# Kernel optimization log

Hardware: AMD Instinct MI355X
Metric: run time of the kernel (lower is better)

Reference implementation:

```python
import jax, jax.numpy as jnp
import numpy as np

C = 1024
H = 16
DH = C // H
T = 2048
B = 2
EPS = 1e-5


def setup_inputs() -> dict:
    key = jax.random.key(0)
    ks = jax.random.split(key, 11)
    s = 1.0 / np.sqrt(C)
    return {
        "x": jax.random.normal(ks[0], (B, C, T), dtype=jnp.float32),
        "Wq": jax.random.normal(ks[1], (C, C), dtype=jnp.float32) * s,
        "bq": jax.random.normal(ks[2], (C,), dtype=jnp.float32) * 0.01,
        "Wk": jax.random.normal(ks[3], (C, C), dtype=jnp.float32) * s,
        "bk": jax.random.normal(ks[4], (C,), dtype=jnp.float32) * 0.01,
        "Wv": jax.random.normal(ks[5], (C, C), dtype=jnp.float32) * s,
        "bv": jax.random.normal(ks[6], (C,), dtype=jnp.float32) * 0.01,
        "Wo": jax.random.normal(ks[7], (C, C), dtype=jnp.float32) * s,
        "bo": jax.random.normal(ks[8], (C,), dtype=jnp.float32) * 0.01,
        "gamma": jax.random.normal(ks[9], (C,), dtype=jnp.float32) * 0.1,
        "beta": jax.random.normal(ks[10], (C,), dtype=jnp.float32) * 0.1,
    }


def reference(x, Wq, bq, Wk, bk, Wv, bv, Wo, bo, gamma, beta):
    scale = DH ** (-0.5)
    # conv1x1 projections: [B,C,T] x [C_out,C_in] -> [B,C,T]
    q = jnp.einsum('bct,dc->bdt', x, Wq) + bq[None, :, None]
    k = jnp.einsum('bct,dc->bdt', x, Wk) + bk[None, :, None]
    v = jnp.einsum('bct,dc->bdt', x, Wv) + bv[None, :, None]
    # split heads: [B,C,T] -> [B,H,Dh,T]
    q = q.reshape(B, H, DH, T).transpose(0, 1, 3, 2) * scale  # [B,H,T,Dh]
    k = k.reshape(B, H, DH, T)                                # [B,H,Dh,T]
    v = v.reshape(B, H, DH, T).transpose(0, 1, 3, 2)          # [B,H,T,Dh]
    sim = jnp.einsum('bhtd,bhds->bhts', q, k)                 # [B,H,T,T]
    attn = jax.nn.softmax(sim, axis=-1)
    attn = jnp.nan_to_num(attn, nan=0.0)
    out = jnp.einsum('bhts,bhsd->bhtd', attn, v)              # [B,H,T,Dh]
    out = out.transpose(0, 1, 3, 2).reshape(B, C, T)          # [B,C,T]
    y = jnp.einsum('bct,dc->bdt', out, Wo) + bo[None, :, None]
    # BatchNorm1d (training mode: batch statistics over B and T)
    mean = jnp.mean(y, axis=(0, 2), keepdims=True)
    var = jnp.var(y, axis=(0, 2), keepdims=True)
    y = (y - mean) * jax.lax.rsqrt(var + EPS)
    y = y * gamma[None, :, None] + beta[None, :, None]
    return x + y
```

## Files before the change

kernel.cpp:

```cpp
#include <hip/hip_runtime.h>

#define CC 1024
#define HH 16
#define DHH 64
#define TT 2048
#define BB 2

typedef short s8v __attribute__((ext_vector_type(8)));
typedef float f32x4 __attribute__((ext_vector_type(4)));
typedef float f32x16 __attribute__((ext_vector_type(16)));

__device__ __forceinline__ unsigned short f2bf(float f) {
    union { float f; unsigned int u; } v; v.f = f;
    unsigned int r = v.u + 0x7FFFu + ((v.u >> 16) & 1u);
    return (unsigned short)(r >> 16);
}

__device__ __forceinline__ float fexp2(float x) {
#if __has_builtin(__builtin_amdgcn_exp2f)
    return __builtin_amdgcn_exp2f(x);
#else
    return exp2f(x);
#endif
}

__device__ __forceinline__ void gl_lds16(const unsigned short* g, unsigned short* l) {
    __builtin_amdgcn_global_load_lds(
        (const __attribute__((address_space(1))) unsigned int*)g,
        (__attribute__((address_space(3))) unsigned int*)l, 16, 0, 0);
}

__device__ __forceinline__ s8v lds_ld(const unsigned short* base, int byteoff) {
    return *(const s8v*)((const char*)base + byteoff);
}

__device__ __forceinline__ int xcd_swz(int orig, int nwg) {
    int cpx = nwg >> 3;
    return (orig & 7) * cpx + (orig >> 3);
}

__global__ void transpose_cast(const float* __restrict__ x, unsigned short* __restrict__ xT) {
    __shared__ float tile[32][33];
    int b = blockIdx.z;
    int t0 = blockIdx.x * 32, c0 = blockIdx.y * 32;
    int tx = threadIdx.x, ty = threadIdx.y;
    const float* xb = x + (size_t)b * CC * TT;
    #pragma unroll
    for (int i = 0; i < 32; i += 8)
        tile[ty + i][tx] = xb[(size_t)(c0 + ty + i) * TT + t0 + tx];
    __syncthreads();
    unsigned short* xTb = xT + (size_t)b * TT * CC;
    #pragma unroll
    for (int i = 0; i < 32; i += 8)
        xTb[(size_t)(t0 + ty + i) * CC + c0 + tx] = f2bf(tile[tx][ty + i]);
}

__global__ void cast_weights(const float* __restrict__ Wq, const float* __restrict__ Wk,
                             const float* __restrict__ Wv, const float* __restrict__ Wo,
                             unsigned short* __restrict__ out) {
    int i = blockIdx.x * 256 + threadIdx.x;
    int which = i >> 18;
    int j = (i & 0x3FFFF) * 4;
    const float* s = (which == 0) ? Wq : (which == 1) ? Wk : (which == 2) ? Wv : Wo;
    float4 v = *(const float4*)(s + j);
    unsigned short* d = out + (size_t)which * 1048576 + j;
    ushort4 pk; pk.x = f2bf(v.x); pk.y = f2bf(v.y); pk.z = f2bf(v.z); pk.w = f2bf(v.w);
    *(ushort4*)d = pk;
}

template<int NFRAG>
__device__ __forceinline__ void gemm_core_k1024(
    const unsigned short* __restrict__ A, const unsigned short* __restrict__ Bt,
    unsigned short* As, unsigned short* Bs,
    int m0, int n0, int tid, f32x4 (&acc)[4][NFRAG]) {
    const int w = tid >> 6, l = tid & 63;
    const int ln = l & 15, hi = l >> 4;
    const int wm = (w >> 1) * 64, wn = (w & 1) * (NFRAG * 16);
    const int BSZ = NFRAG * 1024;
    int offA[4], offB[NFRAG];
    #pragma unroll
    for (int i = 0; i < 4; ++i) {
        int ra = wm + 16 * i + ln;
        offA[i] = ra * 64 + ((hi ^ ((ra >> 1) & 3)) * 16);
    }
    #pragma unroll
    for (int j = 0; j < NFRAG; ++j) {
        int rb = wn + 16 * j + ln;
        offB[j] = rb * 64 + ((hi ^ ((rb >> 1) & 3)) * 16);
    }
    const unsigned short* ap[2];
    const unsigned short* bp[NFRAG / 2];
    #pragma unroll
    for (int j = 0; j < 2; ++j) {
        int p = j * 256 + tid;
        int r = p >> 2, g = (p & 3) ^ ((r >> 1) & 3);
        ap[j] = A + (size_t)(m0 + r) * CC + 8 * g;
    }
    #pragma unroll
    for (int j = 0; j < NFRAG / 2; ++j) {
        int p = j * 256 + tid;
        int r = p >> 2, g = (p & 3) ^ ((r >> 1) & 3);
        bp[j] = Bt + (size_t)(n0 + r) * CC + 8 * g;
    }
    auto stage = [&](int buf) {
        #pragma unroll
        for (int j = 0; j < 2; ++j) {
            gl_lds16(ap[j], As + buf * 4096 + (j * 256 + w * 64) * 8);
            ap[j] += 32;
        }
        #pragma unroll
        for (int j = 0; j < NFRAG / 2; ++j) {
            gl_lds16(bp[j], Bs + buf * BSZ + (j * 256 + w * 64) * 8);
            bp[j] += 32;
        }
    };
    stage(0); stage(1); stage(2);
    if constexpr (NFRAG == 4) asm volatile("s_waitcnt vmcnt(8)" ::: "memory");
    else                      asm volatile("s_waitcnt vmcnt(6)" ::: "memory");
    __builtin_amdgcn_sched_barrier(0);
    __builtin_amdgcn_s_barrier();
    __builtin_amdgcn_sched_barrier(0);
    int buf = 0;
    for (int kk = 0; kk < 32; ++kk) {
        const unsigned short* Ab = As + buf * 4096;
        const unsigned short* Bb = Bs + buf * BSZ;
        s8v a[4], bb[NFRAG];
        #pragma unroll
        for (int i = 0; i < 4; ++i) a[i] = lds_ld(Ab, offA[i]);
        #pragma unroll
        for (int j = 0; j < NFRAG; ++j) bb[j] = lds_ld(Bb, offB[j]);
        __builtin_amdgcn_s_setprio(1);
        #pragma unroll
        for (int i = 0; i < 4; ++i)
            #pragma unroll
            for (int jj = 0; jj < NFRAG; ++jj)
                acc[i][jj] = __builtin_amdgcn_mfma_f32_16x16x32_bf16(a[i], bb[jj], acc[i][jj], 0, 0, 0);
        __builtin_amdgcn_s_setprio(0);
        if (kk < 31) {
            if (kk < 29) {
                if constexpr (NFRAG == 4) asm volatile("s_waitcnt vmcnt(4)" ::: "memory");
                else                      asm volatile("s_waitcnt vmcnt(3)" ::: "memory");
            } else {
                asm volatile("s_waitcnt vmcnt(0)" ::: "memory");
            }
            __builtin_amdgcn_sched_barrier(0);
            __builtin_amdgcn_s_barrier();
            __builtin_amdgcn_sched_barrier(0);
            if (kk < 29) stage(buf);
            buf = (buf == 2) ? 0 : buf + 1;
        }
    }
}

__global__ __launch_bounds__(256, 3)
void gemm_qkv(const unsigned short* __restrict__ xT, const unsigned short* __restrict__ Wb,
              unsigned short* __restrict__ qTp, unsigned short* __restrict__ kTp,
              unsigned short* __restrict__ vp,
              const float* __restrict__ bq, const float* __restrict__ bk,
              const float* __restrict__ bv, float qscale) {
    __shared__ unsigned short As[3 * 4096];
    __shared__ unsigned short Bs[3 * 4096];
    const int tid = threadIdx.x;
    const int wgid = xcd_swz(blockIdx.x, 768);
    const int z = wgid >> 7, bx = wgid & 127;
    const int which = z >> 1, b = z & 1;
    const long TC = (long)TT * CC;

    const unsigned short* A; const unsigned short* Bt;
    int m0, n0;
    if (which < 2) {
        A = xT + (size_t)b * TC;
        Bt = Wb + (size_t)which * 1048576;
        n0 = (bx & 7) * 128; m0 = (bx >> 3) * 128;
    } else {
        A = Wb + 2097152;
        Bt = xT + (size_t)b * TC;
        n0 = (bx & 15) * 128; m0 = (bx >> 4) * 128;
    }

    f32x4 acc[4][4] = {};
    gemm_core_k1024<4>(A, Bt, As, Bs, m0, n0, tid, acc);

    const int w = tid >> 6, l = tid & 63;
    const int ln = l & 15, hi = l >> 4;
    const int wm = (w >> 1) * 64, wn = (w & 1) * 64;

    if (which < 2) {
        unsigned short* Out = (which == 0 ? qTp : kTp) + (size_t)b * TC;
        const float* bias = (which == 0) ? bq : bk;
        float scale = (which == 0) ? qscale : 1.0f;
        #pragma unroll
        for (int i = 0; i < 4; ++i)
            #pragma unroll
            for (int jj = 0; jj < 4; ++jj) {
                int col = n0 + wn + 16 * jj + ln;
                float bvv = bias[col];
                #pragma unroll
                for (int r = 0; r < 4; ++r) {
                    int row = m0 + wm + 16 * i + hi * 4 + r;
                    Out[(size_t)row * CC + col] = f2bf((acc[i][jj][r] + bvv) * scale);
                }
            }
    } else {
        unsigned short* Out = vp + (size_t)b * TC;
        #pragma unroll
        for (int i = 0; i < 4; ++i)
            #pragma unroll
            for (int r = 0; r < 4; ++r) {
                int row = m0 + wm + 16 * i + hi * 4 + r;
                float bvv = bv[row];
                #pragma unroll
                for (int jj = 0; jj < 4; ++jj) {
                    int col = n0 + wn + 16 * jj + ln;
                    Out[(size_t)row * TT + col] = f2bf(acc[i][jj][r] + bvv);
                }
            }
    }
}

__global__ __launch_bounds__(256, 2)
void gemm_y(const unsigned short* __restrict__ Wo, const unsigned short* __restrict__ outT,
            float* __restrict__ y, const float* __restrict__ bo) {
    __shared__ unsigned short As[3 * 4096];
    __shared__ unsigned short Bs[3 * 2048];
    const int tid = threadIdx.x;
    const int wgid = xcd_swz(blockIdx.x, 512);
    const int b = wgid >> 8, bx = wgid & 255;
    const int n0 = (bx & 31) * 64, m0 = (bx >> 5) * 128;
    const long TC = (long)TT * CC;

    f32x4 acc[4][2] = {};
    gemm_core_k1024<2>(Wo, outT + (size_t)b * TC, As, Bs, m0, n0, tid, acc);

    const int w = tid >> 6, l = tid & 63;
    const int ln = l & 15, hi = l >> 4;
    const int wm = (w >> 1) * 64, wn = (w & 1) * 32;
    float* Out = y + (size_t)b * TC;
    #pragma unroll
    for (int i = 0; i < 4; ++i)
        #pragma unroll
        for (int r = 0; r < 4; ++r) {
            int row = m0 + wm + 16 * i + hi * 4 + r;
            float bvv = bo[row];
            #pragma unroll
            for (int jj = 0; jj < 2; ++jj) {
                int col = n0 + wn + 16 * jj + ln;
                Out[(size_t)row * TT + col] = acc[i][jj][r] + bvv;
            }
        }
}

__global__ __launch_bounds__(256, 2)
void attn_kernel(const unsigned short* __restrict__ qT,
                 const unsigned short* __restrict__ kT,
                 const unsigned short* __restrict__ vv,
                 unsigned short* __restrict__ oT) {
    __shared__ unsigned short Ks[2][128 * 64];
    __shared__ unsigned short Vs[2][64 * 128];

    const int tid = threadIdx.x;
    const int w = tid >> 6, l = tid & 63;
    const int l31 = l & 31, h5 = l >> 5, l7 = l & 7;
    const int wgid = xcd_swz(blockIdx.x, 512);
    const int qt0 = (wgid & 15) * 128;
    const int bh = wgid >> 4;
    const int b = bh >> 4, h = bh & 15;
    const size_t bTT = (size_t)b * TT;

    const unsigned short* kp[4];
    const unsigned short* vp2[4];
    #pragma unroll
    for (int j = 0; j < 4; ++j) {
        int c = j * 256 + tid;
        int rk = c >> 3, gk = (c & 7) ^ (rk & 7);
        kp[j] = kT + (bTT + rk) * CC + h * DHH + 8 * gk;
        int rv = c >> 4, gv = (c & 15) ^ (rv & 7);
        vp2[j] = vv + ((size_t)b * CC + h * DHH + rv) * TT + 8 * gv;
    }
    auto stage = [&](int buf) {
        #pragma unroll
        for (int j = 0; j < 4; ++j)
            gl_lds16(kp[j], &Ks[buf][(j * 256 + w * 64) * 8]);
        #pragma unroll
        for (int j = 0; j < 4; ++j)
            gl_lds16(vp2[j], &Vs[buf][(j * 256 + w * 64) * 8]);
        #pragma unroll
        for (int j = 0; j < 4; ++j) { kp[j] += 128 * CC; vp2[j] += 128; }
    };

    stage(0);
    stage(1);

    s8v qf[4];
    {
        const unsigned short* qbase = qT + (bTT + qt0 + w * 32 + l31) * CC + h * DHH + h5 * 8;
        #pragma unroll
        for (int kk = 0; kk < 4; ++kk)
            qf[kk] = *(const s8v*)(qbase + kk * 16);
    }

    int choff[8];
    #pragma unroll
    for (int i = 0; i < 8; ++i) choff[i] = ((2 * i + h5) ^ l7) * 16;
    int rkb[4], rvb[2];
    #pragma unroll
    for (int cb = 0; cb < 4; ++cb) rkb[cb] = (32 * cb + l31) * 128;
    #pragma unroll
    for (int db = 0; db < 2; ++db) rvb[db] = (32 * db + l31) * 256;

    f32x16 sf[4];
    f32x16 of[2] = {};
    float li = 0.f;

    asm volatile("s_waitcnt vmcnt(8)" ::: "memory");
    __builtin_amdgcn_sched_barrier(0);
    __builtin_amdgcn_s_barrier();
    __builtin_amdgcn_sched_barrier(0);

    auto qk = [&](int buf) {
        const unsigned short* Kb = &Ks[buf][0];
        __builtin_amdgcn_s_setprio(1);
        #pragma unroll
        for (int cb = 0; cb < 4; ++cb) {
            f32x16 t = {};
            #pragma unroll
            for (int kk = 0; kk < 4; ++kk) {
                s8v kf = lds_ld(Kb, rkb[cb] + choff[kk]);
                t = __builtin_amdgcn_mfma_f32_32x32x16_bf16(kf, qf[kk], t, 0, 0, 0);
            }
            sf[cb] = t;
        }
        __builtin_amdgcn_s_setprio(0);
    };

    qk(0);

    unsigned int pw[16][2];
    for (int ti = 0; ti < 16; ++ti) {
        {
            float ps = 0.f;
            #pragma unroll
            for (int cb = 0; cb < 4; ++cb)
                #pragma unroll
                for (int q3 = 0; q3 < 4; ++q3) {
                    float p0 = fexp2(sf[cb][4 * q3 + 0]);
                    float p1 = fexp2(sf[cb][4 * q3 + 1]);
                    float p2 = fexp2(sf[cb][4 * q3 + 2]);
                    float p3 = fexp2(sf[cb][4 * q3 + 3]);
                    ps += (p0 + p1) + (p2 + p3);
                    unsigned int w0, w1;
                    asm("v_cvt_pk_bf16_f32 %0, %1, %2" : "=v"(w0) : "v"(p0), "v"(p1));
                    asm("v_cvt_pk_bf16_f32 %0, %1, %2" : "=v"(w1) : "v"(p2), "v"(p3));
                    pw[4 * cb + q3][0] = w0;
                    pw[4 * cb + q3][1] = w1;
                }
            li += ps;
        }

        {
            const unsigned short* Vb = &Vs[ti & 1][0];
            #pragma unroll
            for (int ks = 0; ks < 8; ++ks) {
                unsigned int X0 = pw[2 * ks][0], Y0 = pw[2 * ks + 1][0];
                unsigned int X1 = pw[2 * ks][1], Y1 = pw[2 * ks + 1][1];
                asm("v_permlane32_swap_b32 %0, %1" : "+v"(X0), "+v"(Y0));
                asm("v_permlane32_swap_b32 %0, %1" : "+v"(X1), "+v"(Y1));
                union { unsigned int u[4]; s8v v; } up;
                up.u[0] = X0; up.u[1] = X1; up.u[2] = Y0; up.u[3] = Y1;
                s8v pa = up.v;
                s8v vb0 = lds_ld(Vb, rvb[0] + choff[ks]);
                s8v vb1 = lds_ld(Vb, rvb[1] + choff[ks]);
                __builtin_amdgcn_s_setprio(1);
                of[0] = __builtin_amdgcn_mfma_f32_32x32x16_bf16(pa, vb0, of[0], 0, 0, 0);
                of[1] = __builtin_amdgcn_mfma_f32_32x32x16_bf16(pa, vb1, of[1], 0, 0, 0);
                __builtin_amdgcn_s_setprio(0);
            }
        }

        if (ti < 15) {
            asm volatile("s_waitcnt vmcnt(0)" ::: "memory");
            __builtin_amdgcn_sched_barrier(0);
            __builtin_amdgcn_s_barrier();
            __builtin_amdgcn_sched_barrier(0);
            if (ti < 14) stage(ti & 1);
            qk((ti + 1) & 1);
        }
    }

    li += __shfl_xor(li, 32);
    float inv = 1.0f / li;
    #pragma unroll
    for (int q3 = 0; q3 < 4; ++q3)
        #pragma unroll
        for (int s = 0; s < 4; ++s) {
            float iv = __shfl(inv, 8 * q3 + s + 4 * h5);
            int row = qt0 + w * 32 + 8 * q3 + s + 4 * h5;
            size_t base = (bTT + row) * CC + h * DHH + l31;
            oT[base] = f2bf(of[0][4 * q3 + s] * iv);
            oT[base + 32] = f2bf(of[1][4 * q3 + s] * iv);
        }
}

__global__ __launch_bounds__(256)
void bn_apply(const float* __restrict__ x, const float* __restrict__ y,
              const float* __restrict__ gamma, const float* __restrict__ beta,
              float* __restrict__ out) {
    const int c = blockIdx.x;
    const int tid = threadIdx.x;
    const float* y0 = y + (size_t)c * TT;
    const float* y1 = y + (size_t)(CC + c) * TT;

    float s = 0.f, ss = 0.f;
    for (int t = tid * 4; t < TT; t += 1024) {
        float4 a = *(const float4*)(y0 + t);
        float4 d = *(const float4*)(y1 + t);
        s  += (a.x + a.y) + (a.z + a.w) + (d.x + d.y) + (d.z + d.w);
        ss += (a.x * a.x + a.y * a.y) + (a.z * a.z + a.w * a.w)
            + (d.x * d.x + d.y * d.y) + (d.z * d.z + d.w * d.w);
    }
    #pragma unroll
    for (int m = 1; m < 64; m <<= 1) { s += __shfl_xor(s, m); ss += __shfl_xor(ss, m); }
    __shared__ float a1[4], a2[4];
    __shared__ float sMean, sRstd;
    int wv = tid >> 6;
    if ((tid & 63) == 0) { a1[wv] = s; a2[wv] = ss; }
    __syncthreads();
    if (tid == 0) {
        float S = a1[0] + a1[1] + a1[2] + a1[3];
        float SS = a2[0] + a2[1] + a2[2] + a2[3];
        const float inv_n = 1.0f / (BB * TT);
        float mu = S * inv_n;
        sMean = mu;
        sRstd = rsqrtf(SS * inv_n - mu * mu + 1e-5f);
    }
    __syncthreads();
    float a = gamma[c] * sRstd;
    float bb = beta[c] - sMean * a;

    const float* x0 = x + (size_t)c * TT;
    const float* x1 = x + (size_t)(CC + c) * TT;
    float* o0 = out + (size_t)c * TT;
    float* o1 = out + (size_t)(CC + c) * TT;
    for (int t = tid * 4; t < TT; t += 1024) {
        float4 xv = *(const float4*)(x0 + t);
        float4 yv = *(const float4*)(y0 + t);
        float4 o;
        o.x = xv.x + a * yv.x + bb; o.y = xv.y + a * yv.y + bb;
        o.z = xv.z + a * yv.z + bb; o.w = xv.w + a * yv.w + bb;
        *(float4*)(o0 + t) = o;
        xv = *(const float4*)(x1 + t);
        yv = *(const float4*)(y1 + t);
        o.x = xv.x + a * yv.x + bb; o.y = xv.y + a * yv.y + bb;
        o.z = xv.z + a * yv.z + bb; o.w = xv.w + a * yv.w + bb;
        *(float4*)(o1 + t) = o;
    }
}

extern "C" void kernel_launch(void* const* d_in, const int* in_sizes, int n_in,
                              void* d_out, int out_size, void* d_ws, size_t ws_size,
                              hipStream_t stream) {
    const float* x     = (const float*)d_in[0];
    const float* Wq    = (const float*)d_in[1];
    const float* bq    = (const float*)d_in[2];
    const float* Wk    = (const float*)d_in[3];
    const float* bk    = (const float*)d_in[4];
    const float* Wv    = (const float*)d_in[5];
    const float* bv    = (const float*)d_in[6];
    const float* Wo    = (const float*)d_in[7];
    const float* bo    = (const float*)d_in[8];
    const float* gamma = (const float*)d_in[9];
    const float* beta  = (const float*)d_in[10];
    float* out = (float*)d_out;

    char* ws = (char*)d_ws;
    unsigned short* buf0 = (unsigned short*)(ws);
    unsigned short* Wb   = (unsigned short*)(ws + 8388608);
    unsigned short* qTp  = (unsigned short*)(ws + 16777216);
    unsigned short* kTp  = (unsigned short*)(ws + 25165824);
    unsigned short* vp   = (unsigned short*)(ws + 33554432);
    float* yp            = (float*)(ws + 16777216);

    transpose_cast<<<dim3(TT / 32, CC / 32, BB), dim3(32, 8), 0, stream>>>(x, buf0);
    cast_weights<<<dim3(4096), dim3(256), 0, stream>>>(Wq, Wk, Wv, Wo, Wb);

    gemm_qkv<<<dim3(768), dim3(256), 0, stream>>>(
        buf0, Wb, qTp, kTp, vp, bq, bk, bv, 0.125f * 1.4426950408889634f);

    attn_kernel<<<dim3(512), dim3(256), 0, stream>>>(qTp, kTp, vp, buf0);

    gemm_y<<<dim3(512), dim3(256), 0, stream>>>(Wb + 3145728, buf0, yp, bo);

    bn_apply<<<dim3(CC), dim3(256), 0, stream>>>(x, yp, gamma, beta, out);
}
```

Before: 119.3 us.

## Interleave softmax exp with PV MFMAs and cache y in LDS for BN apply

The attention loop now converts each 32-column block of scores to bf16 probabilities and immediately issues the matching PV MFMAs, instead of computing all probabilities before any PV work. Two independent accumulator chains per output half break the MFMA dependency, and they are summed at the end. The first QK MFMA uses a zero constant operand rather than a zeroed temporary. Separately, bn_apply keeps the y rows it reads for the statistics in shared memory so the apply pass does not reload them from global memory. The extra accumulators raise register pressure and the 16 KB shared buffer may lower bn_apply occupancy.

```diff
diff --git a/kernel.cpp b/kernel.cpp
--- a/kernel.cpp
+++ b/kernel.cpp
@@ -308,8 +308,9 @@
     #pragma unroll
     for (int db = 0; db < 2; ++db) rvb[db] = (32 * db + l31) * 256;
 
+    const f32x16 fzero = {};
     f32x16 sf[4];
-    f32x16 of[2] = {};
+    f32x16 of0a = {}, of0b = {}, of1a = {}, of1b = {};
     float li = 0.f;
 
     asm volatile("s_waitcnt vmcnt(8)" ::: "memory");
@@ -322,9 +323,10 @@
         __builtin_amdgcn_s_setprio(1);
         #pragma unroll
         for (int cb = 0; cb < 4; ++cb) {
-            f32x16 t = {};
+            s8v kf0 = lds_ld(Kb, rkb[cb] + choff[0]);
+            f32x16 t = __builtin_amdgcn_mfma_f32_32x32x16_bf16(kf0, qf[0], fzero, 0, 0, 0);
             #pragma unroll
-            for (int kk = 0; kk < 4; ++kk) {
+            for (int kk = 1; kk < 4; ++kk) {
                 s8v kf = lds_ld(Kb, rkb[cb] + choff[kk]);
                 t = __builtin_amdgcn_mfma_f32_32x32x16_bf16(kf, qf[kk], t, 0, 0, 0);
             }
@@ -335,47 +337,52 @@
 
     qk(0);
 
-    unsigned int pw[16][2];
     for (int ti = 0; ti < 16; ++ti) {
-        {
-            float ps = 0.f;
+        const unsigned short* Vb = &Vs[ti & 1][0];
+        float ps = 0.f;
+        #pragma unroll
+        for (int cb = 0; cb < 4; ++cb) {
+            unsigned int w8[4][2];
             #pragma unroll
-            for (int cb = 0; cb < 4; ++cb)
-                #pragma unroll
-                for (int q3 = 0; q3 < 4; ++q3) {
-                    float p0 = fexp2(sf[cb][4 * q3 + 0]);
-                    float p1 = fexp2(sf[cb][4 * q3 + 1]);
-                    float p2 = fexp2(sf[cb][4 * q3 + 2]);
-                    float p3 = fexp2(sf[cb][4 * q3 + 3]);
-                    ps += (p0 + p1) + (p2 + p3);
-                    unsigned int w0, w1;
-                    asm("v_cvt_pk_bf16_f32 %0, %1, %2" : "=v"(w0) : "v"(p0), "v"(p1));
-                    asm("v_cvt_pk_bf16_f32 %0, %1, %2" : "=v"(w1) : "v"(p2), "v"(p3));
-                    pw[4 * cb + q3][0] = w0;
-                    pw[4 * cb + q3][1] = w1;
-                }
-            li += ps;
-        }
-
-        {
-            const unsigned short* Vb = &Vs[ti & 1][0];
-            #pragma unroll
-            for (int ks = 0; ks < 8; ++ks) {
-                unsigned int X0 = pw[2 * ks][0], Y0 = pw[2 * ks + 1][0];
-                unsigned int X1 = pw[2 * ks][1], Y1 = pw[2 * ks + 1][1];
+            for (int q3 = 0; q3 < 4; ++q3) {
+                float p0 = fexp2(sf[cb][4 * q3 + 0]);
+                float p1 = fexp2(sf[cb][4 * q3 + 1]);
+                float p2 = fexp2(sf[cb][4 * q3 + 2]);
+                float p3 = fexp2(sf[cb][4 * q3 + 3]);
+                ps += (p0 + p1) + (p2 + p3);
+                asm("v_cvt_pk_bf16_f32 %0, %1, %2" : "=v"(w8[q3][0]) : "v"(p0), "v"(p1));
+                asm("v_cvt_pk_bf16_f32 %0, %1, %2" : "=v"(w8[q3][1]) : "v"(p2), "v"(p3));
+            }
+            {
+                unsigned int X0 = w8[0][0], Y0 = w8[1][0];
+                unsigned int X1 = w8[0][1], Y1 = w8[1][1];
                 asm("v_permlane32_swap_b32 %0, %1" : "+v"(X0), "+v"(Y0));
                 asm("v_permlane32_swap_b32 %0, %1" : "+v"(X1), "+v"(Y1));
                 union { unsigned int u[4]; s8v v; } up;
                 up.u[0] = X0; up.u[1] = X1; up.u[2] = Y0; up.u[3] = Y1;
-                s8v pa = up.v;
-                s8v vb0 = lds_ld(Vb, rvb[0] + choff[ks]);
-                s8v vb1 = lds_ld(Vb, rvb[1] + choff[ks]);
+                s8v vb0 = lds_ld(Vb, rvb[0] + choff[2 * cb]);
+                s8v vb1 = lds_ld(Vb, rvb[1] + choff[2 * cb]);
                 __builtin_amdgcn_s_setprio(1);
-                of[0] = __builtin_amdgcn_mfma_f32_32x32x16_bf16(pa, vb0, of[0], 0, 0, 0);
-                of[1] = __builtin_amdgcn_mfma_f32_32x32x16_bf16(pa, vb1, of[1], 0, 0, 0);
+                of0a = __builtin_amdgcn_mfma_f32_32x32x16_bf16(up.v, vb0, of0a, 0, 0, 0);
+                of1a = __builtin_amdgcn_mfma_f32_32x32x16_bf16(up.v, vb1, of1a, 0, 0, 0);
                 __builtin_amdgcn_s_setprio(0);
             }
-        }
+            {
+                unsigned int X0 = w8[2][0], Y0 = w8[3][0];
+                unsigned int X1 = w8[2][1], Y1 = w8[3][1];
+                asm("v_permlane32_swap_b32 %0, %1" : "+v"(X0), "+v"(Y0));
+                asm("v_permlane32_swap_b32 %0, %1" : "+v"(X1), "+v"(Y1));
+                union { unsigned int u[4]; s8v v; } up;
+                up.u[0] = X0; up.u[1] = X1; up.u[2] = Y0; up.u[3] = Y1;
+                s8v vb0 = lds_ld(Vb, rvb[0] + choff[2 * cb + 1]);
+                s8v vb1 = lds_ld(Vb, rvb[1] + choff[2 * cb + 1]);
+                __builtin_amdgcn_s_setprio(1);
+                of0b = __builtin_amdgcn_mfma_f32_32x32x16_bf16(up.v, vb0, of0b, 0, 0, 0);
+                of1b = __builtin_amdgcn_mfma_f32_32x32x16_bf16(up.v, vb1, of1b, 0, 0, 0);
+                __builtin_amdgcn_s_setprio(0);
+            }
+        }
+        li += ps;
 
         if (ti < 15) {
             asm volatile("s_waitcnt vmcnt(0)" ::: "memory");
@@ -387,6 +394,8 @@
         }
     }
 
+    f32x16 o0 = of0a + of0b;
+    f32x16 o1 = of1a + of1b;
     li += __shfl_xor(li, 32);
     float inv = 1.0f / li;
     #pragma unroll
@@ -396,8 +405,8 @@
             float iv = __shfl(inv, 8 * q3 + s + 4 * h5);
             int row = qt0 + w * 32 + 8 * q3 + s + 4 * h5;
             size_t base = (bTT + row) * CC + h * DHH + l31;
-            oT[base] = f2bf(of[0][4 * q3 + s] * iv);
-            oT[base + 32] = f2bf(of[1][4 * q3 + s] * iv);
+            oT[base] = f2bf(o0[4 * q3 + s] * iv);
+            oT[base + 32] = f2bf(o1[4 * q3 + s] * iv);
         }
 }
 
@@ -405,6 +414,7 @@
 void bn_apply(const float* __restrict__ x, const float* __restrict__ y,
               const float* __restrict__ gamma, const float* __restrict__ beta,
               float* __restrict__ out) {
+    __shared__ float ys[2][TT];
     const int c = blockIdx.x;
     const int tid = threadIdx.x;
     const float* y0 = y + (size_t)c * TT;
@@ -414,6 +424,8 @@
     for (int t = tid * 4; t < TT; t += 1024) {
         float4 a = *(const float4*)(y0 + t);
         float4 d = *(const float4*)(y1 + t);
+        *(float4*)(&ys[0][t]) = a;
+        *(float4*)(&ys[1][t]) = d;
         s  += (a.x + a.y) + (a.z + a.w) + (d.x + d.y) + (d.z + d.w);
         ss += (a.x * a.x + a.y * a.y) + (a.z * a.z + a.w * a.w)
             + (d.x * d.x + d.y * d.y) + (d.z * d.z + d.w * d.w);
@@ -443,13 +455,13 @@
     float* o1 = out + (size_t)(CC + c) * TT;
     for (int t = tid * 4; t < TT; t += 1024) {
         float4 xv = *(const float4*)(x0 + t);
-        float4 yv = *(const float4*)(y0 + t);
+        float4 yv = *(const float4*)(&ys[0][t]);
         float4 o;
         o.x = xv.x + a * yv.x + bb; o.y = xv.y + a * yv.y + bb;
         o.z = xv.z + a * yv.z + bb; o.w = xv.w + a * yv.w + bb;
         *(float4*)(o0 + t) = o;
         xv = *(const float4*)(x1 + t);
-        yv = *(const float4*)(y1 + t);
+        yv = *(const float4*)(&ys[1][t]);
         o.x = xv.x + a * yv.x + bb; o.y = xv.y + a * yv.y + bb;
         o.z = xv.z + a * yv.z + bb; o.w = xv.w + a * yv.w + bb;
         *(float4*)(o1 + t) = o;
```

Measured after the change: 117.9 us. About the same (-1.2%).
